# Kernel optimization log

Hardware: AMD Instinct MI355X
Metric: run time of the kernel (lower is better)

## Reference

```python
import jax, jax.numpy as jnp
import numpy as np

N_QUBITS = 14
DEPTH = 2
DIM = 2 ** N_QUBITS
BATCH = 2048
INPUT_DIM = 784
NUM_CLASSES = 10
N_FEATURES = N_QUBITS + N_QUBITS * (N_QUBITS - 1) // 2  # 105


def _make_signs():
    # qubit 0 is the most significant bit of the flattened statevector index
    bits = (np.arange(DIM)[None, :] >> (N_QUBITS - 1 - np.arange(N_QUBITS))[:, None]) & 1
    z = (1.0 - 2.0 * bits).astype(np.float32)  # (n_qubits, DIM): Z eigenvalues per basis state
    rows = [z[i] for i in range(N_QUBITS)]
    for i in range(N_QUBITS):
        for j in range(i + 1, N_QUBITS):
            rows.append(z[i] * z[j])
    return np.stack(rows)  # (N_FEATURES, DIM)

SIGNS = _make_signs()


def _cnot(state, ctrl, tgt):
    # state: (batch, 2, 2, ..., 2); qubit q lives on axis q+1
    ca = ctrl + 1
    s0 = jnp.take(state, 0, axis=ca)
    s1 = jnp.take(state, 1, axis=ca)
    t_ax = tgt + 1 if tgt < ctrl else tgt  # target axis after control axis removed
    s1 = jnp.flip(s1, axis=t_ax)           # X on target where control = 1
    return jnp.stack([s0, s1], axis=ca)


def setup_inputs() -> dict:
    key = jax.random.key(0)
    ks = jax.random.split(key, 3)
    return {
        "x": jax.random.normal(ks[0], (BATCH, INPUT_DIM), jnp.float32),
        "proj_w": jax.random.normal(ks[1], (N_QUBITS, INPUT_DIM), jnp.float32) * 0.03,
        "proj_b": jnp.zeros((N_QUBITS,), jnp.float32),
        "cls_w": jax.random.normal(ks[2], (NUM_CLASSES, N_FEATURES), jnp.float32) * 0.1,
        "cls_b": jnp.zeros((NUM_CLASSES,), jnp.float32),
    }


def reference(x, proj_w, proj_b, cls_w, cls_b):
    b = x.shape[0]
    # classical pre-processing: Linear -> tanh * pi (rotation angles)
    angles = jnp.tanh(x @ proj_w.T + proj_b) * jnp.pi  # (B, n_qubits)
    half = 0.5 * angles
    cos_h, sin_h = jnp.cos(half), jnp.sin(half)
    # RY(theta) on |0> = [cos(t/2), sin(t/2)]; layer of RYs gives a product state
    state = jnp.ones((b,) + (1,) * N_QUBITS, x.dtype)
    for q in range(N_QUBITS):
        shape = (b,) + (1,) * q + (2,) + (1,) * (N_QUBITS - q - 1)
        amp = jnp.stack([cos_h[:, q], sin_h[:, q]], axis=1).reshape(shape)
        state = state * amp
    # chain-topology CNOT entangling layers (all-real gates -> real statevector)
    for _ in range(DEPTH):
        for i in range(N_QUBITS - 1):
            state = _cnot(state, i, i + 1)
    probs = jnp.square(state).reshape(b, DIM)  # |psi|^2
    # <Z_i> and <Z_i Z_j> as one GEMM against precomputed sign rows
    feats = probs @ jnp.asarray(SIGNS).T  # (B, N_FEATURES)
    return feats @ cls_w.T + cls_b
```

## Files before the change

kernel.cpp:

```cpp
#include <hip/hip_runtime.h>
#include <math.h>

#define BATCH 2048
#define IN_DIM 784
#define NQ 14
#define NF 105
#define NC 10


__device__ __forceinline__ unsigned zmask(int q) {
    return (0x1555u << (q & 1)) & ((2u << q) - 1u);
}

template <int CTRL>
__device__ __forceinline__ float dppadd(float x) {
    return x + __int_as_float(__builtin_amdgcn_update_dpp(
        0, __float_as_int(x), CTRL, 0xF, 0xF, true));
}

__device__ __forceinline__ float wave_allreduce(float x, int xor32addr) {
    x = dppadd<0xB1>(x);
    x = dppadd<0x4E>(x);
    x = dppadd<0x141>(x);
    x = dppadd<0x140>(x);
    x = x + __int_as_float(__builtin_amdgcn_ds_swizzle(__float_as_int(x), 0x401F));
#if __has_builtin(__builtin_amdgcn_permlane32_swap)
    {
        typedef unsigned u2v __attribute__((ext_vector_type(2)));
        u2v r = __builtin_amdgcn_permlane32_swap(
            (unsigned)__float_as_int(x), (unsigned)__float_as_int(x), false, false);
        x = __int_as_float((int)r[0]) + __int_as_float((int)r[1]);
    }
#else
    x = x + __int_as_float(__builtin_amdgcn_ds_bpermute(xor32addr, __float_as_int(x)));
#endif
    return x;
}

__global__ __launch_bounds__(256) void qfm_kernel(
    const float* __restrict__ x,
    const float* __restrict__ pw,
    const float* __restrict__ pb,
    const float* __restrict__ cw,
    const float* __restrict__ cb,
    float* __restrict__ out)
{
    const int wave = (int)((blockIdx.x * blockDim.x + threadIdx.x) >> 6);
    const int lane = (int)(threadIdx.x & 63);
    const int xor32addr = ((lane ^ 32) << 2);

    const float4* xr4 = reinterpret_cast<const float4*>(x + (size_t)wave * IN_DIM);
    float4 xv[3];
#pragma unroll
    for (int k = 0; k < 3; ++k) xv[k] = xr4[lane + 64 * k];
    float4 xrem = make_float4(0.f, 0.f, 0.f, 0.f);
    if (lane < 4) xrem = xr4[192 + lane];

    float acc[NQ];
#pragma unroll
    for (int q = 0; q < NQ; ++q) {
        const float4* wr4 = reinterpret_cast<const float4*>(pw + (size_t)q * IN_DIM);
        float a = 0.f;
#pragma unroll
        for (int k = 0; k < 3; ++k) {
            float4 wv = wr4[lane + 64 * k];
            a += xv[k].x * wv.x + xv[k].y * wv.y + xv[k].z * wv.z + xv[k].w * wv.w;
        }
        if (lane < 4) {
            float4 wv = wr4[192 + lane];
            a += xrem.x * wv.x + xrem.y * wv.y + xrem.z * wv.z + xrem.w * wv.w;
        }
        acc[q] = a;
    }

#pragma unroll
    for (int q = 0; q < NQ; ++q) acc[q] = wave_allreduce(acc[q], xor32addr);

    float c[NQ];
#pragma unroll
    for (int q = 0; q < NQ; ++q) {
        const float a = acc[q] + pb[q];
        const float e = __expf(2.0f * a);
        const float r = __builtin_amdgcn_rcpf(e + 1.0f);
        const float t = fmaf(-2.0f, r, 1.0f);
        c[q] = __cosf(3.14159265358979323846f * t);
    }

    float acc_out[NC];
#pragma unroll
    for (int k = 0; k < NC; ++k) acc_out[k] = 0.f;

#pragma unroll
    for (int rep = 0; rep < 2; ++rep) {
        const int f = lane + rep * 64;
        if (f < NF) {
            unsigned m;
            if (f < NQ) {
                m = zmask(f);
            } else {
                const int g = f - NQ;
                const float sq = __builtin_amdgcn_sqrtf(182.25f - 2.0f * (float)g);
                const int i = (int)(13.5f - sq + 1.0e-4f);
                const int j = i + 1 + g - (i * (27 - i)) / 2;
                m = zmask(i) ^ zmask(j);
            }
            float prod = 1.f;
#pragma unroll
            for (int q = 0; q < NQ; ++q) {
                const float mult = ((m >> q) & 1u) ? c[q] : 1.0f;
                prod *= mult;
            }
#pragma unroll
            for (int k = 0; k < NC; ++k)
                acc_out[k] += cw[k * NF + f] * prod;
        }
    }

    float myout = 0.f;
#pragma unroll
    for (int k = 0; k < NC; ++k) {
        const float a = wave_allreduce(acc_out[k], xor32addr);
        if (lane == k) myout = a + cb[k];
    }
    if (lane < NC) out[(size_t)wave * NC + lane] = myout;
}

extern "C" void kernel_launch(void* const* d_in, const int* in_sizes, int n_in,
                              void* d_out, int out_size, void* d_ws, size_t ws_size,
                              hipStream_t stream) {
    const float* x  = (const float*)d_in[0];
    const float* pw = (const float*)d_in[1];
    const float* pb = (const float*)d_in[2];
    const float* cw = (const float*)d_in[3];
    const float* cb = (const float*)d_in[4];
    float* out = (float*)d_out;

    qfm_kernel<<<dim3(BATCH / 4), dim3(256), 0, stream>>>(x, pw, pb, cw, cb, out);
}
```

Baseline: 13.22 us.

## Split each row's projection dot product across two waves with LDS combine

Each batch row is now handled by two waves, each covering half of the 784-element input and projection weights, so 2 rows go to each 256-thread block instead of 4. The partial 14-qubit sums are exchanged through shared memory after a block barrier, and then one wave per row finishes the feature and classifier stage while the other exits. This aims to shorten the per-wave load and dot-product latency and double the number of waves in flight. The cost is a block barrier, an LDS round trip, and idle waves during the second phase.

Result: slower. 14.08 us (+6.5%).

```diff
diff --git a/kernel.cpp b/kernel.cpp
--- a/kernel.cpp
+++ b/kernel.cpp
@@ -6,6 +6,7 @@
 #define NQ 14
 #define NF 105
 #define NC 10
+#define HALF_CHUNKS 98
 
 
 __device__ __forceinline__ unsigned zmask(int q) {
@@ -45,30 +46,32 @@
     const float* __restrict__ cb,
     float* __restrict__ out)
 {
-    const int wave = (int)((blockIdx.x * blockDim.x + threadIdx.x) >> 6);
-    const int lane = (int)(threadIdx.x & 63);
+    const int t    = (int)threadIdx.x;
+    const int lane = t & 63;
+    const int wv   = t >> 6;
+    const int rb   = wv >> 1;
+    const int half = wv & 1;
+    const int row  = (int)blockIdx.x * 2 + rb;
     const int xor32addr = ((lane ^ 32) << 2);
 
-    const float4* xr4 = reinterpret_cast<const float4*>(x + (size_t)wave * IN_DIM);
-    float4 xv[3];
-#pragma unroll
-    for (int k = 0; k < 3; ++k) xv[k] = xr4[lane + 64 * k];
-    float4 xrem = make_float4(0.f, 0.f, 0.f, 0.f);
-    if (lane < 4) xrem = xr4[192 + lane];
+    __shared__ __align__(16) float part[2][2][16];
+
+    const float4* xr4 = reinterpret_cast<const float4*>(x + (size_t)row * IN_DIM)
+                        + half * HALF_CHUNKS;
+    const float4 xv0 = xr4[lane];
+    float4 xv1 = make_float4(0.f, 0.f, 0.f, 0.f);
+    if (lane < HALF_CHUNKS - 64) xv1 = xr4[64 + lane];
 
     float acc[NQ];
 #pragma unroll
     for (int q = 0; q < NQ; ++q) {
-        const float4* wr4 = reinterpret_cast<const float4*>(pw + (size_t)q * IN_DIM);
-        float a = 0.f;
-#pragma unroll
-        for (int k = 0; k < 3; ++k) {
-            float4 wv = wr4[lane + 64 * k];
-            a += xv[k].x * wv.x + xv[k].y * wv.y + xv[k].z * wv.z + xv[k].w * wv.w;
-        }
-        if (lane < 4) {
-            float4 wv = wr4[192 + lane];
-            a += xrem.x * wv.x + xrem.y * wv.y + xrem.z * wv.z + xrem.w * wv.w;
+        const float4* wr4 = reinterpret_cast<const float4*>(pw + (size_t)q * IN_DIM)
+                            + half * HALF_CHUNKS;
+        const float4 w0 = wr4[lane];
+        float a = xv0.x * w0.x + xv0.y * w0.y + xv0.z * w0.z + xv0.w * w0.w;
+        if (lane < HALF_CHUNKS - 64) {
+            const float4 w1 = wr4[64 + lane];
+            a += xv1.x * w1.x + xv1.y * w1.y + xv1.z * w1.z + xv1.w * w1.w;
         }
         acc[q] = a;
     }
@@ -76,14 +79,36 @@
 #pragma unroll
     for (int q = 0; q < NQ; ++q) acc[q] = wave_allreduce(acc[q], xor32addr);
 
+    if (lane == 0) {
+        float4* p4 = reinterpret_cast<float4*>(&part[rb][half][0]);
+        p4[0] = make_float4(acc[0], acc[1], acc[2],  acc[3]);
+        p4[1] = make_float4(acc[4], acc[5], acc[6],  acc[7]);
+        p4[2] = make_float4(acc[8], acc[9], acc[10], acc[11]);
+        reinterpret_cast<float2*>(&part[rb][half][12])[0] = make_float2(acc[12], acc[13]);
+    }
+    __syncthreads();
+    if (half) return;
+
+    const float4* a4 = reinterpret_cast<const float4*>(&part[rb][0][0]);
+    const float4* b4 = reinterpret_cast<const float4*>(&part[rb][1][0]);
+    const float4 s0 = a4[0], s1 = a4[1], s2 = a4[2];
+    const float4 t0 = b4[0], t1 = b4[1], t2 = b4[2];
+    const float2 s3 = reinterpret_cast<const float2*>(&part[rb][0][12])[0];
+    const float2 t3 = reinterpret_cast<const float2*>(&part[rb][1][12])[0];
+    float sum[NQ] = {
+        s0.x + t0.x, s0.y + t0.y, s0.z + t0.z, s0.w + t0.w,
+        s1.x + t1.x, s1.y + t1.y, s1.z + t1.z, s1.w + t1.w,
+        s2.x + t2.x, s2.y + t2.y, s2.z + t2.z, s2.w + t2.w,
+        s3.x + t3.x, s3.y + t3.y };
+
     float c[NQ];
 #pragma unroll
     for (int q = 0; q < NQ; ++q) {
-        const float a = acc[q] + pb[q];
+        const float a = sum[q] + pb[q];
         const float e = __expf(2.0f * a);
         const float r = __builtin_amdgcn_rcpf(e + 1.0f);
-        const float t = fmaf(-2.0f, r, 1.0f);
-        c[q] = __cosf(3.14159265358979323846f * t);
+        const float tt = fmaf(-2.0f, r, 1.0f);
+        c[q] = __cosf(3.14159265358979323846f * tt);
     }
 
     float acc_out[NC];
@@ -122,7 +147,7 @@
         const float a = wave_allreduce(acc_out[k], xor32addr);
         if (lane == k) myout = a + cb[k];
     }
-    if (lane < NC) out[(size_t)wave * NC + lane] = myout;
+    if (lane < NC) out[(size_t)row * NC + lane] = myout;
 }
 
 extern "C" void kernel_launch(void* const* d_in, const int* in_sizes, int n_in,
@@ -135,5 +160,5 @@
     const float* cb = (const float*)d_in[4];
     float* out = (float*)d_out;
 
-    qfm_kernel<<<dim3(BATCH / 4), dim3(256), 0, stream>>>(x, pw, pb, cw, cb, out);
+    qfm_kernel<<<dim3(BATCH / 2), dim3(256), 0, stream>>>(x, pw, pb, cw, cb, out);
 }
```
